# Kernel optimization log

Hardware: AMD Instinct MI355X
Metric: run time of the kernel (lower is better)

## Reference

```python
import jax, jax.numpy as jnp
import numpy as np

D_MODEL = 256
N_HEADS = 8
N_LEVELS = 4
N_POINTS = 4
HEAD_DIM = D_MODEL // N_HEADS
SPATIAL = [(64, 64), (32, 32), (16, 16), (8, 8)]
LEN_IN = sum(h * w for h, w in SPATIAL)
BATCH = 4
LEN_Q = LEN_IN


def _offset_bias():
    # replicate the module's _reset_parameters grid init for sampling_offsets.bias
    th = np.arange(N_HEADS, dtype=np.float64) * (2.0 * np.pi / N_HEADS)
    g = np.stack([np.cos(th), np.sin(th)], -1)
    g = g / np.abs(g).max(-1, keepdims=True)
    g = np.tile(g[:, None, None, :], (1, N_LEVELS, N_POINTS, 1))
    g = g * (np.arange(N_POINTS) + 1)[None, None, :, None]
    return jnp.asarray(g.reshape(-1), jnp.float32)


def setup_inputs() -> dict:
    key = jax.random.key(0)
    ks = jax.random.split(key, 10)
    s = 1.0 / np.sqrt(D_MODEL)
    return {
        "query": jax.random.normal(ks[0], (BATCH, LEN_Q, D_MODEL), jnp.float32),
        "reference_points": jax.random.uniform(ks[1], (BATCH, LEN_Q, N_LEVELS, 2), jnp.float32),
        "input_flatten": jax.random.normal(ks[2], (BATCH, LEN_IN, D_MODEL), jnp.float32),
        "input_spatial_shapes": np.array(SPATIAL, dtype=np.int64),
        "input_level_start_index": np.cumsum([0] + [h * w for h, w in SPATIAL[:-1]]).astype(np.int64),
        "W_val": jax.random.normal(ks[3], (D_MODEL, D_MODEL), jnp.float32) * s,
        "b_val": jnp.zeros((D_MODEL,), jnp.float32),
        "W_off": jax.random.normal(ks[4], (D_MODEL, N_HEADS * N_LEVELS * N_POINTS * 2), jnp.float32) * 0.01,
        "b_off": _offset_bias(),
        "W_attn": jax.random.normal(ks[5], (D_MODEL, N_HEADS * N_LEVELS * N_POINTS), jnp.float32) * 0.01,
        "b_attn": jnp.zeros((N_HEADS * N_LEVELS * N_POINTS,), jnp.float32),
        "W_out": jax.random.normal(ks[6], (D_MODEL, D_MODEL), jnp.float32) * s,
        "b_out": jnp.zeros((D_MODEL,), jnp.float32),
    }


def bilinear_sample(v, grid):
    # v: [B, C, H, W]; grid: [B, Q, P, 2] normalized to [-1, 1] (x=W axis, y=H axis)
    # matches torch F.grid_sample(mode='bilinear', padding_mode='zeros', align_corners=False)
    B, C, H, W = v.shape
    x = (grid[..., 0] + 1.0) * (W * 0.5) - 0.5
    y = (grid[..., 1] + 1.0) * (H * 0.5) - 0.5
    x0 = jnp.floor(x)
    y0 = jnp.floor(y)
    wx = x - x0
    wy = y - y0
    v_flat = v.reshape(B, C, H * W)

    def corner(xi, yi, wgt):
        valid = (xi >= 0) & (xi <= W - 1) & (yi >= 0) & (yi <= H - 1)
        xc = jnp.clip(xi, 0, W - 1).astype(jnp.int32)
        yc = jnp.clip(yi, 0, H - 1).astype(jnp.int32)
        idx = (yc * W + xc).reshape(B, 1, -1)
        g = jnp.take_along_axis(v_flat, jnp.broadcast_to(idx, (B, C, idx.shape[-1])), axis=2)
        return g * (wgt * valid).reshape(B, 1, -1)

    out = (corner(x0, y0, (1 - wx) * (1 - wy))
           + corner(x0 + 1, y0, wx * (1 - wy))
           + corner(x0, y0 + 1, (1 - wx) * wy)
           + corner(x0 + 1, y0 + 1, wx * wy))
    return out.reshape(B, C, grid.shape[1], grid.shape[2])


def reference(query, reference_points, input_flatten, input_spatial_shapes,
              input_level_start_index, W_val, b_val, W_off, b_off,
              W_attn, b_attn, W_out, b_out):
    ss = np.asarray(input_spatial_shapes)  # static [L, 2] (H, W)
    Nb, Lq, _ = query.shape
    value = (input_flatten @ W_val + b_val).reshape(Nb, -1, N_HEADS, HEAD_DIM)
    off = (query @ W_off + b_off).reshape(Nb, Lq, N_HEADS, N_LEVELS, N_POINTS, 2)
    attn = (query @ W_attn + b_attn).reshape(Nb, Lq, N_HEADS, N_LEVELS * N_POINTS)
    attn = jax.nn.softmax(attn, -1).reshape(Nb, Lq, N_HEADS, N_LEVELS, N_POINTS)
    # offset normalizer: (W, H) per level
    normalizer = jnp.asarray(ss[:, ::-1].copy(), jnp.float32)
    loc = reference_points[:, :, None, :, None, :] + off / normalizer[None, None, None, :, None, :]
    grids = 2.0 * loc - 1.0  # [N, Lq, H, L, P, 2]
    splits = np.cumsum([int(h) * int(w) for h, w in ss])[:-1]
    value_list = jnp.split(value, splits, axis=1)
    out = jnp.zeros((Nb * N_HEADS, HEAD_DIM, Lq), query.dtype)
    for lid, (h, w) in enumerate(ss):
        h, w = int(h), int(w)
        v = value_list[lid].transpose(0, 2, 3, 1).reshape(Nb * N_HEADS, HEAD_DIM, h, w)
        g = grids[:, :, :, lid].transpose(0, 2, 1, 3, 4).reshape(Nb * N_HEADS, Lq, N_POINTS, 2)
        sampled = bilinear_sample(v, g)  # [N*H, D, Lq, P]
        aw = attn[:, :, :, lid].transpose(0, 2, 1, 3).reshape(Nb * N_HEADS, 1, Lq, N_POINTS)
        out = out + (sampled * aw).sum(-1)
    out = out.reshape(Nb, N_HEADS * HEAD_DIM, Lq).transpose(0, 2, 1)
    return out @ W_out + b_out
```

## Files before the change

### kernel.cpp

```cpp
#include <hip/hip_runtime.h>
#include <hip/hip_bf16.h>
#include <math.h>

typedef unsigned short ushort_t;
typedef __attribute__((ext_vector_type(8))) short bf16x8;
typedef __attribute__((ext_vector_type(4))) float f32x4;
typedef __attribute__((ext_vector_type(2))) float f32x2;

constexpr int BATCH   = 4;
constexpr int D_MODEL = 256;
constexpr int LEN_IN  = 5440;
constexpr int LEN_Q   = 5440;
constexpr int M_TOT   = BATCH * LEN_Q;

#define ASG __attribute__((address_space(1)))
#define ASL __attribute__((address_space(3)))

__device__ __forceinline__ void gld16(const void* g, void* l) {
    __builtin_amdgcn_global_load_lds((ASG const void*)g, (ASL void*)l, 16, 0, 0);
}

__device__ __forceinline__ ushort_t bfbits(float x) {
    __hip_bfloat16 h = __float2bfloat16(x);
    ushort_t u; __builtin_memcpy(&u, &h, 2); return u;
}
__device__ __forceinline__ unsigned pk2(float a, float b) {
    return (unsigned)bfbits(a) | ((unsigned)bfbits(b) << 16);
}

__global__ __launch_bounds__(256) void pack_weights(
    const float* __restrict__ Wv, const float* __restrict__ Wout,
    const float* __restrict__ Wo, const float* __restrict__ Wa,
    const float* __restrict__ b_off, const float* __restrict__ b_attn,
    ushort_t* __restrict__ wvT, ushort_t* __restrict__ woutT,
    ushort_t* __restrict__ woaT, float* __restrict__ bias_oa)
{
    const int blk = blockIdx.x, t = threadIdx.x;
    if (blk < 64) {
        const float* src = (blk < 32) ? Wv : Wout;
        ushort_t*    dst = (blk < 32) ? wvT : woutT;
        const int k0 = (blk & 31) * 8;
        float f[8];
#pragma unroll
        for (int i = 0; i < 8; i++) f[i] = src[(k0 + i) * 256 + t];
        *(uint4*)(dst + t * 256 + k0) =
            make_uint4(pk2(f[0], f[1]), pk2(f[2], f[3]),
                       pk2(f[4], f[5]), pk2(f[6], f[7]));
    } else if (blk < 96) {
        const int k0 = (blk - 64) * 8;
#pragma unroll
        for (int rep = 0; rep < 2; rep++) {
            const int j = (rep == 0) ? t : 256 + t;
            if (rep == 1 && t >= 128) break;
            float f[8];
#pragma unroll
            for (int i = 0; i < 8; i++)
                f[i] = (j < 256) ? Wo[(k0 + i) * 256 + j]
                                 : Wa[(k0 + i) * 128 + (j - 256)];
            *(uint4*)(woaT + j * 256 + k0) =
                make_uint4(pk2(f[0], f[1]), pk2(f[2], f[3]),
                           pk2(f[4], f[5]), pk2(f[6], f[7]));
        }
    } else {
        bias_oa[t] = b_off[t];
        if (t < 128) bias_oa[256 + t] = b_attn[t];
    }
}

template <int OUT_MODE, bool A_F32, int NB>
__device__ __forceinline__ void gemm_core(
    const void* __restrict__ Ap, const ushort_t* __restrict__ BT,
    const float* __restrict__ bias, void* __restrict__ Cp, int N,
    int bm, int bn, ushort_t* As, ushort_t* Bs)
{
    const int tid  = threadIdx.x;
    const int wave = tid >> 6, lane = tid & 63;
    const int wm = (wave >> 1) * 64, wn = (wave & 1) * 64;
    const int c0 = 2 * wave, c1 = 2 * wave + 1;
    const int kb = (lane & 3) * 8;
    const int ar0 = bm + c0 * 16 + (lane >> 2);
    const int ar1 = bm + c1 * 16 + (lane >> 2);
    const ushort_t* gA0h = nullptr; const ushort_t* gA1h = nullptr;
    const float*    gA0f = nullptr; const float*    gA1f = nullptr;
    if (A_F32) {
        gA0f = (const float*)Ap + (size_t)ar0 * 256 + kb;
        gA1f = (const float*)Ap + (size_t)ar1 * 256 + kb;
    } else {
        gA0h = (const ushort_t*)Ap + (size_t)ar0 * 256 + kb;
        gA1h = (const ushort_t*)Ap + (size_t)ar1 * 256 + kb;
    }
    const ushort_t* gB0[NB]; const ushort_t* gB1[NB];
    ushort_t* lB0[NB]; ushort_t* lB1[NB];
#pragma unroll
    for (int nb = 0; nb < NB; nb++) {
        gB0[nb] = BT + (size_t)(bn + nb * 128 + c0 * 16 + (lane >> 2)) * 256 + kb;
        gB1[nb] = BT + (size_t)(bn + nb * 128 + c1 * 16 + (lane >> 2)) * 256 + kb;
        lB0[nb] = Bs + nb * 4096 + c0 * 512;
        lB1[nb] = Bs + nb * 4096 + c1 * 512;
    }
    ushort_t* lA0 = As + c0 * 512;
    ushort_t* lA1 = As + c1 * 512;

    f32x4 acc[NB][4][4] = {};
    const int row = lane & 15, kg = (lane >> 4) * 8;
    for (int kt = 0; kt < 8; kt++) {
        if (A_F32) {
            float4 a0 = *(const float4*)gA0f;
            float4 a1 = *(const float4*)(gA0f + 4);
            float4 b0 = *(const float4*)gA1f;
            float4 b1 = *(const float4*)(gA1f + 4);
            *(uint4*)(lA0 + lane * 8) =
                make_uint4(pk2(a0.x, a0.y), pk2(a0.z, a0.w),
                           pk2(a1.x, a1.y), pk2(a1.z, a1.w));
            *(uint4*)(lA1 + lane * 8) =
                make_uint4(pk2(b0.x, b0.y), pk2(b0.z, b0.w),
                           pk2(b1.x, b1.y), pk2(b1.z, b1.w));
            gA0f += 32; gA1f += 32;
        } else {
            gld16(gA0h, lA0); gld16(gA1h, lA1);
            gA0h += 32; gA1h += 32;
        }
#pragma unroll
        for (int nb = 0; nb < NB; nb++) {
            gld16(gB0[nb], lB0[nb]); gld16(gB1[nb], lB1[nb]);
            gB0[nb] += 32; gB1[nb] += 32;
        }
        __syncthreads();
        bf16x8 af[4];
#pragma unroll
        for (int i = 0; i < 4; i++)
            af[i] = *(const bf16x8*)(As + (wm + i * 16 + row) * 32 + kg);
#pragma unroll
        for (int nb = 0; nb < NB; nb++) {
            bf16x8 bfr[4];
#pragma unroll
            for (int j = 0; j < 4; j++)
                bfr[j] = *(const bf16x8*)(Bs + nb * 4096 + (wn + j * 16 + row) * 32 + kg);
#pragma unroll
            for (int i = 0; i < 4; i++)
#pragma unroll
                for (int j = 0; j < 4; j++)
                    acc[nb][i][j] = __builtin_amdgcn_mfma_f32_16x16x32_bf16(
                        af[i], bfr[j], acc[nb][i][j], 0, 0, 0);
        }
        __syncthreads();
    }

    const int col = lane & 15, rbase = (lane >> 4) * 4;
#pragma unroll
    for (int nb = 0; nb < NB; nb++) {
#pragma unroll
        for (int j = 0; j < 4; j++) {
            const int cc = bn + nb * 128 + wn + j * 16 + col;
            const float bv = bias[cc];
#pragma unroll
            for (int i = 0; i < 4; i++) {
                const int rr = bm + wm + i * 16 + rbase;
#pragma unroll
                for (int r = 0; r < 4; r++) {
                    const float v = acc[nb][i][j][r] + bv;
                    const int m = rr + r;
                    if (OUT_MODE == 0) {
                        ((float*)Cp)[(size_t)m * N + cc] = v;
                    } else {
                        const int bb  = m / LEN_IN;
                        const int pix = m - bb * LEN_IN;
                        const int head = cc >> 5, ch = cc & 31;
                        ((ushort_t*)Cp)[((size_t)((bb * 8 + head) * LEN_IN + pix) << 5) + ch] = bfbits(v);
                    }
                }
            }
        }
    }
}

__global__ __launch_bounds__(256) void gemm_dual(
    const float* __restrict__ inflat, const ushort_t* __restrict__ wvT,
    const float* __restrict__ b_val, ushort_t* __restrict__ value_bf,
    const float* __restrict__ query, const ushort_t* __restrict__ woaT,
    const float* __restrict__ bias_oa, float* __restrict__ offattn)
{
    __shared__ ushort_t As[128 * 32];
    __shared__ ushort_t Bs[2 * 128 * 32];
    const int blk = blockIdx.x;
    if (blk < 170) {
        gemm_core<2, true, 2>(inflat, wvT, b_val, value_bf, 256,
                              blk * 128, 0, As, Bs);
    } else if (blk < 340) {
        gemm_core<0, true, 2>(query, woaT, bias_oa, offattn, 384,
                              (blk - 170) * 128, 0, As, Bs);
    } else {
        gemm_core<0, true, 1>(query, woaT, bias_oa, offattn, 384,
                              (blk - 340) * 128, 256, As, Bs);
    }
}

__global__ __launch_bounds__(256) void gemm_out(
    const ushort_t* __restrict__ mid_bf, const ushort_t* __restrict__ woutT,
    const float* __restrict__ b_out, float* __restrict__ out)
{
    __shared__ ushort_t As[128 * 32];
    __shared__ ushort_t Bs[128 * 32];
    const int bn = (blockIdx.x & 1) * 128, bm = (blockIdx.x >> 1) * 128;
    gemm_core<0, false, 1>(mid_bf, woutT, b_out, out, 256, bm, bn, As, Bs);
}

__device__ __forceinline__ void accd(f32x2& a, unsigned u, f32x2 w) {
    f32x2 v;
    v.x = __uint_as_float(u << 16);
    v.y = __uint_as_float(u & 0xFFFF0000u);
    a = w * v + a;
}
__device__ __forceinline__ void accp(f32x2* a, uint4 u, float wf) {
    const f32x2 w = {wf, wf};
    accd(a[0], u.x, w); accd(a[1], u.y, w);
    accd(a[2], u.z, w); accd(a[3], u.w, w);
}

__global__ __launch_bounds__(256) void msda_sample_v3(
    const ushort_t* __restrict__ value,
    const float* __restrict__ refp,
    const float* __restrict__ offattn,
    ushort_t* __restrict__ mid)
{
    const int tid = threadIdx.x;
    const unsigned bid = blockIdx.x;
    const int xcd   = bid & 7;
    const int pos   = bid >> 3;
    const int slice = pos / 85;
    const int qc    = pos - slice * 85;
    const int bh    = xcd * 4 + slice;
    const int b     = bh >> 3, h = bh & 7;

    const int ql = tid >> 2;
    const int cg = tid & 3;
    const int bq = b * LEN_Q + qc * 64 + ql;

    const float* oab = offattn + (size_t)bq * 384;
    const float* lp = oab + 256 + h * 16;
    float4 l0 = ((const float4*)lp)[0];
    float4 l1 = ((const float4*)lp)[1];
    float4 l2 = ((const float4*)lp)[2];
    float4 l3 = ((const float4*)lp)[3];
    float lg[16] = {l0.x, l0.y, l0.z, l0.w, l1.x, l1.y, l1.z, l1.w,
                    l2.x, l2.y, l2.z, l2.w, l3.x, l3.y, l3.z, l3.w};
    float mx = lg[0];
#pragma unroll
    for (int j = 1; j < 16; j++) mx = fmaxf(mx, lg[j]);

    const float* op = oab + h * 32;
    const float* rp = refp + (size_t)bq * 8;

    const char* vb = (const char*)value + (size_t)bh * (LEN_IN * 64) + cg * 16;

    f32x2 acc2[4];
#pragma unroll
    for (int d = 0; d < 4; d++) acc2[d] = (f32x2){0.f, 0.f};
    float esum = 0.f;

#pragma unroll
    for (int l = 0; l < 4; l++) {
        const int   shift = 6 - l;
        const int   W     = 1 << shift;
        const float fW    = (float)W;
        const float invW  = __uint_as_float((unsigned)(127 - shift) << 23);
        const int   st    = (l == 0) ? 0 : (l == 1) ? 4096 : (l == 2) ? 5120 : 5376;

        const float2 rl = *(const float2*)(rp + l * 2);
        const float4 oA = ((const float4*)op)[l * 2];
        const float4 oB = ((const float4*)op)[l * 2 + 1];
        const float oxA[4] = {oA.x, oA.z, oB.x, oB.z};
        const float oyA[4] = {oA.y, oA.w, oB.y, oB.w};
#pragma unroll
        for (int p = 0; p < 4; p++) {
            const float x = (rl.x + oxA[p] * invW) * fW - 0.5f;
            const float y = (rl.y + oyA[p] * invW) * fW - 0.5f;
            const float x0f = floorf(x), y0f = floorf(y);
            const float wx = x - x0f, wy = y - y0f;
            const int ix0 = (int)x0f, iy0 = (int)y0f;
            const int ix1 = ix0 + 1,  iy1 = iy0 + 1;
            const float vx0 = (ix0 >= 0 && ix0 < W) ? 1.f : 0.f;
            const float vx1 = (ix1 >= 0 && ix1 < W) ? 1.f : 0.f;
            const float vy0 = (iy0 >= 0 && iy0 < W) ? 1.f : 0.f;
            const float vy1 = (iy1 >= 0 && iy1 < W) ? 1.f : 0.f;
            const int cx0 = min(max(ix0, 0), W - 1);
            const int cx1 = min(max(ix1, 0), W - 1);
            const int cy0 = min(max(iy0, 0), W - 1);
            const int cy1 = min(max(iy1, 0), W - 1);
            const float hx0 = (1.f - wx) * vx0, hx1 = wx * vx1;
            const float hy0 = (1.f - wy) * vy0, hy1 = wy * vy1;

            const float e = __expf(lg[l * 4 + p] - mx);
            esum += e;
            const float w00 = e * hx0 * hy0, w01 = e * hx1 * hy0;
            const float w10 = e * hx0 * hy1, w11 = e * hx1 * hy1;

            const int r0a = st + (cy0 << shift);
            const int r1a = st + (cy1 << shift);
            uint4 v00 = *(const uint4*)(vb + ((size_t)(r0a + cx0) << 6));
            uint4 v01 = *(const uint4*)(vb + ((size_t)(r0a + cx1) << 6));
            uint4 v10 = *(const uint4*)(vb + ((size_t)(r1a + cx0) << 6));
            uint4 v11 = *(const uint4*)(vb + ((size_t)(r1a + cx1) << 6));

            accp(acc2, v00, w00);
            accp(acc2, v01, w01);
            accp(acc2, v10, w10);
            accp(acc2, v11, w11);
        }
    }

    const float inv = 1.f / esum;
    uint4 o;
    o.x = pk2(acc2[0].x * inv, acc2[0].y * inv);
    o.y = pk2(acc2[1].x * inv, acc2[1].y * inv);
    o.z = pk2(acc2[2].x * inv, acc2[2].y * inv);
    o.w = pk2(acc2[3].x * inv, acc2[3].y * inv);
    ((uint4*)(mid + (size_t)bq * 256 + h * 32))[cg] = o;
}

extern "C" void kernel_launch(void* const* d_in, const int* in_sizes, int n_in,
                              void* d_out, int out_size, void* d_ws, size_t ws_size,
                              hipStream_t stream)
{
    const float* query  = (const float*)d_in[0];
    const float* refp   = (const float*)d_in[1];
    const float* inflat = (const float*)d_in[2];
    const float* W_val  = (const float*)d_in[5];
    const float* b_val  = (const float*)d_in[6];
    const float* W_off  = (const float*)d_in[7];
    const float* W_attn = (const float*)d_in[9];
    const float* b_off  = (const float*)d_in[8];
    const float* b_attn = (const float*)d_in[10];
    const float* W_out  = (const float*)d_in[11];
    const float* b_out  = (const float*)d_in[12];
    float* out = (float*)d_out;

    char* ws = (char*)d_ws;
    ushort_t* mid_bf   = (ushort_t*)ws;
    ushort_t* value_bf = (ushort_t*)(ws + 11141120);
    ushort_t* wvT      = (ushort_t*)(ws + 22282240);
    ushort_t* woutT    = (ushort_t*)(ws + 22413312);
    ushort_t* woaT     = (ushort_t*)(ws + 22544384);
    float*    bias_oa  = (float*)   (ws + 22740992);
    float*    offattn  = (float*)   (ws + 22742528);

    dim3 blk(256);
    pack_weights<<<dim3(97), blk, 0, stream>>>(
        W_val, W_out, W_off, W_attn, b_off, b_attn,
        wvT, woutT, woaT, bias_oa);
    gemm_dual<<<dim3(510), blk, 0, stream>>>(
        inflat, wvT, b_val, value_bf, query, woaT, bias_oa, offattn);
    msda_sample_v3<<<dim3(2720), blk, 0, stream>>>(
        value_bf, refp, offattn, mid_bf);
    gemm_out<<<dim3(340), blk, 0, stream>>>(
        mid_bf, woutT, b_out, out);
}
```

Baseline: 184.9 us.

## Compute sampling weights once per point and share via LDS across channel threads

```diff
diff --git a/kernel.cpp b/kernel.cpp
--- a/kernel.cpp
+++ b/kernel.cpp
@@ -217,12 +217,16 @@
     accd(a[2], u.z, w); accd(a[3], u.w, w);
 }
 
-__global__ __launch_bounds__(256) void msda_sample_v3(
+__global__ __launch_bounds__(256) void msda_sample_v4(
     const ushort_t* __restrict__ value,
     const float* __restrict__ refp,
     const float* __restrict__ offattn,
     ushort_t* __restrict__ mid)
 {
+    __shared__ float4 wLDS[64][16];
+    __shared__ float4 aLDS[64][16];
+    __shared__ float  esLDS[64];
+
     const int tid = threadIdx.x;
     const unsigned bid = blockIdx.x;
     const int xcd   = bid & 7;
@@ -231,50 +235,41 @@
     const int qc    = pos - slice * 85;
     const int bh    = xcd * 4 + slice;
     const int b     = bh >> 3, h = bh & 7;
-
-    const int ql = tid >> 2;
-    const int cg = tid & 3;
-    const int bq = b * LEN_Q + qc * 64 + ql;
-
-    const float* oab = offattn + (size_t)bq * 384;
-    const float* lp = oab + 256 + h * 16;
-    float4 l0 = ((const float4*)lp)[0];
-    float4 l1 = ((const float4*)lp)[1];
-    float4 l2 = ((const float4*)lp)[2];
-    float4 l3 = ((const float4*)lp)[3];
-    float lg[16] = {l0.x, l0.y, l0.z, l0.w, l1.x, l1.y, l1.z, l1.w,
-                    l2.x, l2.y, l2.z, l2.w, l3.x, l3.y, l3.z, l3.w};
-    float mx = lg[0];
-#pragma unroll
-    for (int j = 1; j < 16; j++) mx = fmaxf(mx, lg[j]);
-
-    const float* op = oab + h * 32;
-    const float* rp = refp + (size_t)bq * 8;
-
-    const char* vb = (const char*)value + (size_t)bh * (LEN_IN * 64) + cg * 16;
-
-    f32x2 acc2[4];
-#pragma unroll
-    for (int d = 0; d < 4; d++) acc2[d] = (f32x2){0.f, 0.f};
-    float esum = 0.f;
-
-#pragma unroll
-    for (int l = 0; l < 4; l++) {
-        const int   shift = 6 - l;
-        const int   W     = 1 << shift;
-        const float fW    = (float)W;
-        const float invW  = __uint_as_float((unsigned)(127 - shift) << 23);
-        const int   st    = (l == 0) ? 0 : (l == 1) ? 4096 : (l == 2) ? 5120 : 5376;
-
-        const float2 rl = *(const float2*)(rp + l * 2);
-        const float4 oA = ((const float4*)op)[l * 2];
-        const float4 oB = ((const float4*)op)[l * 2 + 1];
-        const float oxA[4] = {oA.x, oA.z, oB.x, oB.z};
-        const float oyA[4] = {oA.y, oA.w, oB.y, oB.w};
-#pragma unroll
-        for (int p = 0; p < 4; p++) {
-            const float x = (rl.x + oxA[p] * invW) * fW - 0.5f;
-            const float y = (rl.y + oyA[p] * invW) * fW - 0.5f;
+    const int bqbase = b * LEN_Q + qc * 64;
+
+    {
+        const int p  = tid & 15;
+        const int qg = tid >> 4;
+        const int l  = p >> 2;
+        const int shift = 6 - l;
+        const int W  = 1 << shift;
+        const float fW   = (float)W;
+        const float invW = __uint_as_float((unsigned)(127 - shift) << 23);
+        const int st = (l == 0) ? 0 : (l == 1) ? 4096 : (l == 2) ? 5120 : 5376;
+
+#pragma unroll
+        for (int it = 0; it < 4; it++) {
+            const int ql = it * 16 + qg;
+            const int bq = bqbase + ql;
+            const float* oab = offattn + (size_t)bq * 384;
+            const float2 off = *(const float2*)(oab + h * 32 + p * 2);
+            const float  lgv = oab[256 + h * 16 + p];
+            const float2 rl  = *(const float2*)(refp + (size_t)bq * 8 + l * 2);
+
+            float mx = lgv;
+            mx = fmaxf(mx, __shfl_xor(mx, 1));
+            mx = fmaxf(mx, __shfl_xor(mx, 2));
+            mx = fmaxf(mx, __shfl_xor(mx, 4));
+            mx = fmaxf(mx, __shfl_xor(mx, 8));
+            const float e = __expf(lgv - mx);
+            float es = e;
+            es += __shfl_xor(es, 1);
+            es += __shfl_xor(es, 2);
+            es += __shfl_xor(es, 4);
+            es += __shfl_xor(es, 8);
+
+            const float x = (rl.x + off.x * invW) * fW - 0.5f;
+            const float y = (rl.y + off.y * invW) * fW - 0.5f;
             const float x0f = floorf(x), y0f = floorf(y);
             const float wx = x - x0f, wy = y - y0f;
             const int ix0 = (int)x0f, iy0 = (int)y0f;
@@ -290,26 +285,49 @@
             const float hx0 = (1.f - wx) * vx0, hx1 = wx * vx1;
             const float hy0 = (1.f - wy) * vy0, hy1 = wy * vy1;
 
-            const float e = __expf(lg[l * 4 + p] - mx);
-            esum += e;
-            const float w00 = e * hx0 * hy0, w01 = e * hx1 * hy0;
-            const float w10 = e * hx0 * hy1, w11 = e * hx1 * hy1;
-
-            const int r0a = st + (cy0 << shift);
-            const int r1a = st + (cy1 << shift);
-            uint4 v00 = *(const uint4*)(vb + ((size_t)(r0a + cx0) << 6));
-            uint4 v01 = *(const uint4*)(vb + ((size_t)(r0a + cx1) << 6));
-            uint4 v10 = *(const uint4*)(vb + ((size_t)(r1a + cx0) << 6));
-            uint4 v11 = *(const uint4*)(vb + ((size_t)(r1a + cx1) << 6));
-
-            accp(acc2, v00, w00);
-            accp(acc2, v01, w01);
-            accp(acc2, v10, w10);
-            accp(acc2, v11, w11);
-        }
-    }
-
-    const float inv = 1.f / esum;
+            const int off00 = (st + (cy0 << shift) + cx0) << 6;
+            const int dxB   = (cx1 - cx0) << 6;
+            const int dyB   = ((cy1 - cy0) << shift) << 6;
+
+            const int ps = p ^ (ql & 15);
+            wLDS[ql][ps] = make_float4(e * hx0 * hy0, e * hx1 * hy0,
+                                       e * hx0 * hy1, e * hx1 * hy1);
+            aLDS[ql][ps] = make_float4(__int_as_float(off00), __int_as_float(dxB),
+                                       __int_as_float(dyB), 0.f);
+            if (p == 0) esLDS[ql] = es;
+        }
+    }
+    __syncthreads();
+
+    const int ql = tid >> 2;
+    const int cg = tid & 3;
+    const int bq = bqbase + ql;
+    const char* vb = (const char*)value + (size_t)bh * (LEN_IN * 64) + cg * 16;
+    const float inv = 1.f / esLDS[ql];
+    const int qs = ql & 15;
+
+    f32x2 acc2[4];
+#pragma unroll
+    for (int d = 0; d < 4; d++) acc2[d] = (f32x2){0.f, 0.f};
+
+#pragma unroll
+    for (int pp = 0; pp < 16; pp++) {
+        const float4 w  = wLDS[ql][pp ^ qs];
+        const float4 ai = aLDS[ql][pp ^ qs];
+        const int o00 = __float_as_int(ai.x);
+        const int dx  = __float_as_int(ai.y);
+        const int dy  = __float_as_int(ai.z);
+        const char* c00 = vb + o00;
+        uint4 v00 = *(const uint4*)(c00);
+        uint4 v01 = *(const uint4*)(c00 + dx);
+        uint4 v10 = *(const uint4*)(c00 + dy);
+        uint4 v11 = *(const uint4*)(c00 + dx + dy);
+        accp(acc2, v00, w.x);
+        accp(acc2, v01, w.y);
+        accp(acc2, v10, w.z);
+        accp(acc2, v11, w.w);
+    }
+
     uint4 o;
     o.x = pk2(acc2[0].x * inv, acc2[0].y * inv);
     o.y = pk2(acc2[1].x * inv, acc2[1].y * inv);
@@ -350,7 +368,7 @@
         wvT, woutT, woaT, bias_oa);
     gemm_dual<<<dim3(510), blk, 0, stream>>>(
         inflat, wvT, b_val, value_bf, query, woaT, bias_oa, offattn);
-    msda_sample_v3<<<dim3(2720), blk, 0, stream>>>(
+    msda_sample_v4<<<dim3(2720), blk, 0, stream>>>(
         value_bf, refp, offattn, mid_bf);
     gemm_out<<<dim3(340), blk, 0, stream>>>(
         mid_bf, woutT, b_out, out);
```

Result: faster. 176.7 us (-4.4%).
